# Kernel tuning notes

Hardware: AMD Instinct MI355X
Metric: run time of the kernel (lower is better)

The kernel has to match this reference:

```python
import jax, jax.numpy as jnp
import numpy as np

D_MODEL = 1024
H = 16
D_K = D_MODEL // H


def setup_inputs() -> dict:
    key = jax.random.key(0)
    ks = jax.random.split(key, 12)
    B, S = 4, 2048
    q = jax.random.normal(ks[0], (B, S, D_MODEL), jnp.float32)
    k = jax.random.normal(ks[1], (B, S, D_MODEL), jnp.float32)
    v = jax.random.normal(ks[2], (B, S, D_MODEL), jnp.float32)
    # causal mask, broadcastable to [B, H, S, S]; mask==0 positions are blocked
    mask = jnp.tril(jnp.ones((S, S), jnp.int32))[None, None]
    scale = 1.0 / np.sqrt(D_MODEL)
    Wq = jax.random.normal(ks[3], (D_MODEL, D_MODEL), jnp.float32) * scale
    bq = jax.random.normal(ks[4], (D_MODEL,), jnp.float32) * 0.02
    Wk = jax.random.normal(ks[5], (D_MODEL, D_MODEL), jnp.float32) * scale
    bk = jax.random.normal(ks[6], (D_MODEL,), jnp.float32) * 0.02
    Wv = jax.random.normal(ks[7], (D_MODEL, D_MODEL), jnp.float32) * scale
    bv = jax.random.normal(ks[8], (D_MODEL,), jnp.float32) * 0.02
    Wo = jax.random.normal(ks[9], (D_MODEL, D_MODEL), jnp.float32) * scale
    bo = jax.random.normal(ks[10], (D_MODEL,), jnp.float32) * 0.02
    return {"q": q, "k": k, "v": v, "mask": mask,
            "Wq": Wq, "bq": bq, "Wk": Wk, "bk": bk,
            "Wv": Wv, "bv": bv, "Wo": Wo, "bo": bo}


def reference(q, k, v, mask, Wq, bq, Wk, bk, Wv, bv, Wo, bo):
    B, S, _ = q.shape
    # linear projections (torch nn.Linear: x @ W.T + b)
    query = q @ Wq.T + bq
    key = k @ Wk.T + bk
    value = v @ Wv.T + bv
    # [B, S, D] -> [B, H, S, d_k]
    def split_heads(x):
        return x.reshape(B, S, H, D_K).transpose(0, 2, 1, 3)
    query, key, value = split_heads(query), split_heads(key), split_heads(value)
    # scaled dot-product attention, scores: [B, H, S, S]
    scores = jnp.einsum('bhqd,bhkd->bhqk', query, key) / np.sqrt(D_K)
    scores = jnp.where(mask == 0, jnp.float32(-1e9), scores)
    attn = jax.nn.softmax(scores, axis=-1)
    x = jnp.einsum('bhqk,bhkd->bhqd', attn, value)  # [B, H, S, d_k]
    x = x.transpose(0, 2, 1, 3).reshape(B, S, D_MODEL)
    return x @ Wo.T + bo
```

## Files before the change

kernel.cpp:

```cpp
#include <hip/hip_runtime.h>

#define DM 1024
#define SEQ 2048
#define NH 16
#define DK 64

typedef __bf16 bf16x8 __attribute__((ext_vector_type(8)));
typedef float f32x4 __attribute__((ext_vector_type(4)));

#define QSCALE 0.1803368801111244f

__device__ inline unsigned short f2bf(float f) {
    unsigned u = __float_as_uint(f);
    u += 0x7fffu + ((u >> 16) & 1u);
    return (unsigned short)(u >> 16);
}

__device__ inline unsigned pkbf(float lo, float hi) {
    union { __bf16 h[2]; unsigned u; } r;
    r.h[0] = (__bf16)lo; r.h[1] = (__bf16)hi;
    return r.u;
}

__global__ __launch_bounds__(256) void cvt_w(const float* __restrict__ s0,
                                             const float* __restrict__ s1,
                                             const float* __restrict__ s2,
                                             const float* __restrict__ s3,
                                             unsigned short* __restrict__ d0,
                                             unsigned short* __restrict__ d1,
                                             unsigned short* __restrict__ d2,
                                             unsigned short* __restrict__ d3) {
    const float* s;
    unsigned short* d;
    switch (blockIdx.y) {
        case 0: s = s0; d = d0; break;
        case 1: s = s1; d = d1; break;
        case 2: s = s2; d = d2; break;
        default: s = s3; d = d3; break;
    }
    int i = (blockIdx.x * 256 + threadIdx.x) * 4;
    float4 v = *(const float4*)(s + i);
    ushort4 o;
    o.x = f2bf(v.x); o.y = f2bf(v.y); o.z = f2bf(v.z); o.w = f2bf(v.w);
    *(ushort4*)(d + i) = o;
}

__global__ __launch_bounds__(512) void gemm_qkv(
    const float* __restrict__ Aq, const float* __restrict__ Ak,
    const float* __restrict__ Avv,
    const unsigned short* __restrict__ Wq2, const unsigned short* __restrict__ Wk2,
    const unsigned short* __restrict__ Wv2,
    const float* __restrict__ bq2, const float* __restrict__ bk2,
    const float* __restrict__ bv2,
    unsigned short* __restrict__ Cq, unsigned short* __restrict__ Ck,
    unsigned short* __restrict__ Cvt) {
    __shared__ unsigned short lds_a[128 * 64];
    __shared__ unsigned short lds_w[2][128 * 64];

    const int K = DM, N = DM;
    const int t = threadIdx.x;
    const int lane = t & 63;
    const int w = t >> 6;
    const int wr = w >> 1;
    const int wc = w & 1;
    const int seg = blockIdx.x >> 9;
    const int inner = blockIdx.x & 511;
    const int xcd = inner & 7;
    const int idx = inner >> 3;
    const int rowBase = (xcd * 8 + (idx >> 3)) * 128;
    const int colBase = (idx & 7) * 128;
    const int l15 = lane & 15;
    const int lg = lane >> 4;
    const int ar = t >> 2, aq = t & 3;
    const int NIT = K >> 6;

    const float* A = seg == 0 ? Aq : (seg == 1 ? Ak : Avv);
    const unsigned short* W = seg == 0 ? Wq2 : (seg == 1 ? Wk2 : Wv2);
    const float* bias = seg == 0 ? bq2 : (seg == 1 ? bk2 : bv2);

    f32x4 acc[2][4] = {};

    auto STAGE_W = [&](int kt, int buf) {
#pragma unroll
        for (int i = 0; i < 2; ++i) {
            const int row = (w * 2 + i) * 8 + (lane >> 3);
            const int sl = lane & 7;
            const unsigned short* src =
                W + (size_t)(colBase + row) * K + kt * 64 + ((sl ^ (row & 7)) * 8);
            __builtin_amdgcn_global_load_lds(src, &lds_w[buf][(w * 2 + i) * 512], 16, 0, 0);
        }
    };
    auto LOADA = [&](int kt, float4* rf) {
        const float* Af = A + (size_t)(rowBase + ar) * K + kt * 64 + aq * 16;
#pragma unroll
        for (int i = 0; i < 4; ++i) rf[i] = *(const float4*)(Af + i * 4);
    };
    auto WRITEA = [&](const float4* rf) {
#pragma unroll
        for (int i = 0; i < 2; ++i) {
            union { __bf16 h[8]; uint4 u; } pk;
            pk.h[0] = (__bf16)rf[2 * i].x; pk.h[1] = (__bf16)rf[2 * i].y;
            pk.h[2] = (__bf16)rf[2 * i].z; pk.h[3] = (__bf16)rf[2 * i].w;
            pk.h[4] = (__bf16)rf[2 * i + 1].x; pk.h[5] = (__bf16)rf[2 * i + 1].y;
            pk.h[6] = (__bf16)rf[2 * i + 1].z; pk.h[7] = (__bf16)rf[2 * i + 1].w;
            *(uint4*)&lds_a[ar * 64 + (((aq * 2 + i) ^ (ar & 7)) * 8)] = pk.u;
        }
    };
    auto COMPUTE = [&](int wbuf) {
#pragma unroll
        for (int kh = 0; kh < 2; ++kh) {
            bf16x8 af[2], wf[4];
#pragma unroll
            for (int m = 0; m < 2; ++m)
                af[m] = *(const bf16x8*)&lds_a[(wr * 32 + m * 16 + l15) * 64 +
                                               (((kh * 4 + lg) ^ (l15 & 7)) * 8)];
#pragma unroll
            for (int n = 0; n < 4; ++n)
                wf[n] = *(const bf16x8*)&lds_w[wbuf][(wc * 64 + n * 16 + l15) * 64 +
                                                    (((kh * 4 + lg) ^ (l15 & 7)) * 8)];
#pragma unroll
            for (int m = 0; m < 2; ++m)
#pragma unroll
                for (int n = 0; n < 4; ++n)
                    acc[m][n] = __builtin_amdgcn_mfma_f32_16x16x32_bf16(af[m], wf[n],
                                                                        acc[m][n], 0, 0, 0);
        }
    };

    float4 ra[4], rb[4];
    STAGE_W(0, 0);
    LOADA(0, ra);
    for (int kt = 0; kt < NIT; kt += 2) {
        if (kt + 1 < NIT) {
            STAGE_W(kt + 1, 1);
            LOADA(kt + 1, rb);
            asm volatile("s_waitcnt vmcnt(6)" ::: "memory");
        } else {
            asm volatile("s_waitcnt vmcnt(0)" ::: "memory");
        }
        WRITEA(ra);
        asm volatile("s_waitcnt lgkmcnt(0)" ::: "memory");
        __builtin_amdgcn_s_barrier();
        COMPUTE(0);
        __builtin_amdgcn_s_barrier();
        if (kt + 2 < NIT) {
            STAGE_W(kt + 2, 0);
            LOADA(kt + 2, ra);
            asm volatile("s_waitcnt vmcnt(6)" ::: "memory");
        } else {
            asm volatile("s_waitcnt vmcnt(0)" ::: "memory");
        }
        WRITEA(rb);
        asm volatile("s_waitcnt lgkmcnt(0)" ::: "memory");
        __builtin_amdgcn_s_barrier();
        COMPUTE(1);
        __builtin_amdgcn_s_barrier();
    }

    const float oscale = seg == 0 ? QSCALE : 1.0f;
#pragma unroll
    for (int m = 0; m < 2; ++m) {
        int row = rowBase + wr * 32 + m * 16 + lg * 4;
#pragma unroll
        for (int n = 0; n < 4; ++n) {
            int col = colBase + wc * 64 + n * 16 + l15;
            float bv = bias[col];
            if (seg == 2) {
                const int bh = (row >> 11) * NH + (col >> 6);
                const int dloc = col & 63;
                const int s = row & (SEQ - 1);
                ushort4 o;
                o.x = f2bf(acc[m][n][0] + bv);
                o.y = f2bf(acc[m][n][1] + bv);
                o.z = f2bf(acc[m][n][2] + bv);
                o.w = f2bf(acc[m][n][3] + bv);
                *(ushort4*)(Cvt + ((size_t)bh * DK + dloc) * SEQ + s) = o;
            } else {
                unsigned short* C = seg == 0 ? Cq : Ck;
#pragma unroll
                for (int j = 0; j < 4; ++j)
                    C[(size_t)(row + j) * N + col] = f2bf((acc[m][n][j] + bv) * oscale);
            }
        }
    }
}

__global__ __launch_bounds__(512) void gemm_out(const unsigned short* __restrict__ A,
                                                const unsigned short* __restrict__ W,
                                                const float* __restrict__ bias,
                                                float* __restrict__ C) {
    __shared__ unsigned short lds_a[2][128 * 64];
    __shared__ unsigned short lds_w[2][128 * 64];

    const int K = DM, N = DM;
    const int t = threadIdx.x;
    const int lane = t & 63;
    const int w = t >> 6;
    const int wr = w >> 1;
    const int wc = w & 1;
    const int bid = blockIdx.x;
    const int xcd = bid & 7;
    const int idx = bid >> 3;
    const int rowBase = (xcd * 8 + (idx >> 3)) * 128;
    const int colBase = (idx & 7) * 128;
    const int l15 = lane & 15;
    const int lg = lane >> 4;
    const int NIT = K >> 6;

    f32x4 acc[2][4] = {};

    auto STAGE = [&](const unsigned short* M0, unsigned short* ldsb, int kt) {
#pragma unroll
        for (int i = 0; i < 2; ++i) {
            const int row = (w * 2 + i) * 8 + (lane >> 3);
            const int sl = lane & 7;
            const unsigned short* src =
                M0 + (size_t)row * K + kt * 64 + ((sl ^ (row & 7)) * 8);
            __builtin_amdgcn_global_load_lds(src, ldsb + (w * 2 + i) * 512, 16, 0, 0);
        }
    };
    auto COMPUTE = [&](int buf) {
#pragma unroll
        for (int kh = 0; kh < 2; ++kh) {
            bf16x8 af[2], wf[4];
#pragma unroll
            for (int m = 0; m < 2; ++m)
                af[m] = *(const bf16x8*)&lds_a[buf][(wr * 32 + m * 16 + l15) * 64 +
                                                   (((kh * 4 + lg) ^ (l15 & 7)) * 8)];
#pragma unroll
            for (int n = 0; n < 4; ++n)
                wf[n] = *(const bf16x8*)&lds_w[buf][(wc * 64 + n * 16 + l15) * 64 +
                                                   (((kh * 4 + lg) ^ (l15 & 7)) * 8)];
#pragma unroll
            for (int m = 0; m < 2; ++m)
#pragma unroll
                for (int n = 0; n < 4; ++n)
                    acc[m][n] = __builtin_amdgcn_mfma_f32_16x16x32_bf16(af[m], wf[n],
                                                                        acc[m][n], 0, 0, 0);
        }
    };

    const unsigned short* Arow = A + (size_t)rowBase * K;
    const unsigned short* Wrow = W + (size_t)colBase * K;
    STAGE(Wrow, lds_w[0], 0);
    STAGE(Arow, lds_a[0], 0);
    for (int kt = 0; kt < NIT; ++kt) {
        const int cur = kt & 1;
        if (kt + 1 < NIT) {
            STAGE(Wrow, lds_w[cur ^ 1], kt + 1);
            STAGE(Arow, lds_a[cur ^ 1], kt + 1);
            asm volatile("s_waitcnt vmcnt(4)" ::: "memory");
        } else {
            asm volatile("s_waitcnt vmcnt(0)" ::: "memory");
        }
        __builtin_amdgcn_s_barrier();
        COMPUTE(cur);
        __builtin_amdgcn_s_barrier();
    }

#pragma unroll
    for (int m = 0; m < 2; ++m) {
        int row = rowBase + wr * 32 + m * 16 + lg * 4;
#pragma unroll
        for (int n = 0; n < 4; ++n) {
            int col = colBase + wc * 64 + n * 16 + l15;
            float bv = bias[col];
#pragma unroll
            for (int j = 0; j < 4; ++j)
                C[(size_t)(row + j) * N + col] = acc[m][n][j] + bv;
        }
    }
}

__global__ __launch_bounds__(256) void attn(const unsigned short* __restrict__ Q,
                                            const unsigned short* __restrict__ K,
                                            const unsigned short* __restrict__ Vt,
                                            unsigned short* __restrict__ X) {
    __shared__ unsigned short k_lds[2][64 * 64];
    __shared__ unsigned short v_lds[2][64 * 64];

    const int t = threadIdx.x;
    const int lane = t & 63;
    const int w = t >> 6;
    const int l15 = lane & 15, lg = lane >> 4;
    const int c4 = (lane >> 4) & 1, c5 = (lane >> 5) & 1;

    const int orig = blockIdx.x;
    const int flat = (orig & 7) * 128 + (orig >> 3);
    const int bh = flat >> 4;
    const int pr = flat & 15;
    const int b = bh >> 4, h = bh & 15;

    const unsigned short* Qb = Q + (size_t)b * SEQ * DM + h * DK;
    const unsigned short* Kb = K + (size_t)b * SEQ * DM + h * DK;
    const unsigned short* Vb = Vt + (size_t)bh * DK * SEQ;

    const int sr = t >> 3;
    const int sc8 = (t & 7) * 8;
    const int sxo = (sr & 7) * 8;
    const int xork = (l15 & 7) * 8;

    union { unsigned short us[8]; bf16x8 v; } ou;
#pragma unroll
    for (int i = 0; i < 8; ++i) ou.us[i] = 0x3F80;
    const bf16x8 onesf = ou.v;

    bf16x8 kr0, kr1, vr0, vr1;
    int gp = 0;

    auto LOADT = [&](int kv0) {
        kr0 = *(const bf16x8*)(Kb + (size_t)(kv0 + sr) * DM + sc8);
        kr1 = *(const bf16x8*)(Kb + (size_t)(kv0 + 32 + sr) * DM + sc8);
        vr0 = *(const bf16x8*)(Vb + (size_t)sr * SEQ + kv0 + sc8);
        vr1 = *(const bf16x8*)(Vb + (size_t)(32 + sr) * SEQ + kv0 + sc8);
    };

    LOADT(0);

    for (int task = 0; task < 2; ++task) {
        const int qt = task ? 31 - pr : pr;
        const int qrow0 = qt * 64 + w * 16;
        const int qg = qrow0 + l15;

        const bf16x8 qf0 = *(const bf16x8*)(Qb + (size_t)(qrow0 + l15) * DM + lg * 8);
        const bf16x8 qf1 = *(const bf16x8*)(Qb + (size_t)(qrow0 + l15) * DM + lg * 8 + 32);

        f32x4 acc[4] = {};
        f32x4 accS = {};
        const int nt = qt + 1;

        for (int tile = 0; tile < nt; ++tile) {
            const int kv0 = tile << 6;
            unsigned short* kl = k_lds[gp & 1];
            unsigned short* vl = v_lds[gp & 1];
            *(bf16x8*)&kl[sr * 64 + (sc8 ^ sxo)] = kr0;
            *(bf16x8*)&kl[(sr + 32) * 64 + (sc8 ^ sxo)] = kr1;
            *(bf16x8*)&vl[sr * 64 + (sc8 ^ sxo)] = vr0;
            *(bf16x8*)&vl[(sr + 32) * 64 + (sc8 ^ sxo)] = vr1;
            __syncthreads();

            if (tile + 1 < nt)
                LOADT((tile + 1) << 6);
            else if (task == 0)
                LOADT(0);

            f32x4 st[4];
#pragma unroll
            for (int s = 0; s < 4; ++s) {
                const int rb2 = (s * 16 + l15) * 64;
                bf16x8 ka = *(const bf16x8*)&kl[rb2 + ((lg * 8) ^ xork)];
                bf16x8 kb2 = *(const bf16x8*)&kl[rb2 + ((32 + lg * 8) ^ xork)];
                f32x4 z = {};
                z = __builtin_amdgcn_mfma_f32_16x16x32_bf16(ka, qf0, z, 0, 0, 0);
                st[s] = __builtin_amdgcn_mfma_f32_16x16x32_bf16(kb2, qf1, z, 0, 0, 0);
            }

            bf16x8 vf[4][2];
#pragma unroll
            for (int d = 0; d < 4; ++d) {
                const int rb2 = (d * 16 + l15) * 64;
                vf[d][0] = *(const bf16x8*)&vl[rb2 + ((lg * 8) ^ xork)];
                vf[d][1] = *(const bf16x8*)&vl[rb2 + ((32 + lg * 8) ^ xork)];
            }

            float ps[16];
            if (kv0 + 63 > qrow0) {
#pragma unroll
                for (int s = 0; s < 4; ++s)
#pragma unroll
                    for (int j = 0; j < 4; ++j) {
                        const bool ok = kv0 + s * 16 + 4 * lg + j <= qg;
                        ps[s * 4 + j] = ok ? exp2f(st[s][j]) : 0.0f;
                    }
            } else {
#pragma unroll
                for (int s = 0; s < 4; ++s)
#pragma unroll
                    for (int j = 0; j < 4; ++j)
                        ps[s * 4 + j] = exp2f(st[s][j]);
            }

            bf16x8 pf[2];
#pragma unroll
            for (int hh = 0; hh < 2; ++hh) {
                const float* p8 = &ps[hh * 8];
                unsigned wsp[2][2];
#pragma unroll
                for (int s = 0; s < 2; ++s)
#pragma unroll
                    for (int p2 = 0; p2 < 2; ++p2)
                        wsp[s][p2] = pkbf(p8[s * 4 + 2 * p2], p8[s * 4 + 2 * p2 + 1]);
                unsigned n0[2], n1[2];
#pragma unroll
                for (int p2 = 0; p2 < 2; ++p2) {
                    unsigned snd = c5 ? wsp[0][p2] : wsp[1][p2];
                    unsigned exch = __shfl_xor((int)snd, 32, 64);
                    n0[p2] = c5 ? exch : wsp[0][p2];
                    n1[p2] = c5 ? wsp[1][p2] : exch;
                }
                unsigned f0[2], f1[2];
#pragma unroll
                for (int p2 = 0; p2 < 2; ++p2) {
                    unsigned snd = c4 ? n0[p2] : n1[p2];
                    unsigned exch = __shfl_xor((int)snd, 16, 64);
                    f0[p2] = c4 ? exch : n0[p2];
                    f1[p2] = c4 ? n1[p2] : exch;
                }
                union { unsigned u[4]; bf16x8 v; } pu;
                pu.u[0] = f0[0]; pu.u[1] = f0[1]; pu.u[2] = f1[0]; pu.u[3] = f1[1];
                pf[hh] = pu.v;
            }

#pragma unroll
            for (int d = 0; d < 4; ++d) {
                acc[d] = __builtin_amdgcn_mfma_f32_16x16x32_bf16(vf[d][0], pf[0], acc[d], 0, 0, 0);
                acc[d] = __builtin_amdgcn_mfma_f32_16x16x32_bf16(vf[d][1], pf[1], acc[d], 0, 0, 0);
            }
            accS = __builtin_amdgcn_mfma_f32_16x16x32_bf16(onesf, pf[0], accS, 0, 0, 0);
            accS = __builtin_amdgcn_mfma_f32_16x16x32_bf16(onesf, pf[1], accS, 0, 0, 0);
            gp++;
        }

        const float inv = 1.0f / accS[0];
#pragma unroll
        for (int d = 0; d < 4; ++d) {
            ushort4 o;
            o.x = f2bf(acc[d][0] * inv);
            o.y = f2bf(acc[d][1] * inv);
            o.z = f2bf(acc[d][2] * inv);
            o.w = f2bf(acc[d][3] * inv);
            *(ushort4*)&X[(size_t)(b * SEQ + qg) * DM + h * DK + d * 16 + 4 * lg] = o;
        }
    }
}

extern "C" void kernel_launch(void* const* d_in, const int* in_sizes, int n_in,
                              void* d_out, int out_size, void* d_ws, size_t ws_size,
                              hipStream_t stream) {
    const float* q  = (const float*)d_in[0];
    const float* k  = (const float*)d_in[1];
    const float* v  = (const float*)d_in[2];
    const float* Wq = (const float*)d_in[4];
    const float* bq = (const float*)d_in[5];
    const float* Wk = (const float*)d_in[6];
    const float* bk = (const float*)d_in[7];
    const float* Wv = (const float*)d_in[8];
    const float* bv = (const float*)d_in[9];
    const float* Wo = (const float*)d_in[10];
    const float* bo = (const float*)d_in[11];

    const size_t NEL = (size_t)4 * SEQ * DM;
    const size_t WEL = (size_t)DM * DM;
    unsigned short* Qp  = (unsigned short*)d_ws;
    unsigned short* Kp  = Qp + NEL;
    unsigned short* Vp  = Kp + NEL;
    unsigned short* Vt  = Vp + NEL;
    unsigned short* Wob = Vt + NEL;
    unsigned short* Xp  = Vp;
    unsigned short* Wqb = (unsigned short*)d_out;
    unsigned short* Wkb = Wqb + WEL;
    unsigned short* Wvb = Wkb + WEL;

    hipLaunchKernelGGL(cvt_w, dim3(1024, 4), dim3(256), 0, stream, Wq, Wk, Wv, Wo,
                       Wqb, Wkb, Wvb, Wob);
    hipLaunchKernelGGL(gemm_qkv, dim3(1536), dim3(512), 0, stream, q, k, v,
                       Wqb, Wkb, Wvb, bq, bk, bv, Qp, Kp, Vt);
    hipLaunchKernelGGL(attn, dim3(1024), dim3(256), 0, stream, Qp, Kp, Vt, Xp);
    hipLaunchKernelGGL(gemm_out, dim3(512), dim3(512), 0, stream, Xp, Wob, bo,
                       (float*)d_out);
}
```

Measured before the change: 203.7 us.

## Deepen A-operand register prefetch to three stages in QKV projection GEMM

Measured after the change: 201.7 us. Within noise of the previous version (-1.0%).

```diff
diff --git a/kernel.cpp b/kernel.cpp
--- a/kernel.cpp
+++ b/kernel.cpp
@@ -72,7 +72,6 @@
     const int l15 = lane & 15;
     const int lg = lane >> 4;
     const int ar = t >> 2, aq = t & 3;
-    const int NIT = K >> 6;
 
     const float* A = seg == 0 ? Aq : (seg == 1 ? Ak : Avv);
     const unsigned short* W = seg == 0 ? Wq2 : (seg == 1 ? Wk2 : Wv2);
@@ -127,33 +126,26 @@
         }
     };
 
-    float4 ra[4], rb[4];
+    float4 rs[3][4];
     STAGE_W(0, 0);
-    LOADA(0, ra);
-    for (int kt = 0; kt < NIT; kt += 2) {
-        if (kt + 1 < NIT) {
-            STAGE_W(kt + 1, 1);
-            LOADA(kt + 1, rb);
+    LOADA(0, rs[0]);
+    LOADA(1, rs[1]);
+    LOADA(2, rs[2]);
+#pragma unroll
+    for (int kt = 0; kt < 16; ++kt) {
+        if (kt + 1 < 16) STAGE_W(kt + 1, (kt + 1) & 1);
+        if (kt < 14) {
+            asm volatile("s_waitcnt vmcnt(10)" ::: "memory");
+        } else if (kt == 14) {
             asm volatile("s_waitcnt vmcnt(6)" ::: "memory");
         } else {
             asm volatile("s_waitcnt vmcnt(0)" ::: "memory");
         }
-        WRITEA(ra);
+        WRITEA(rs[kt % 3]);
+        if (kt + 3 < 16) LOADA(kt + 3, rs[kt % 3]);
         asm volatile("s_waitcnt lgkmcnt(0)" ::: "memory");
         __builtin_amdgcn_s_barrier();
-        COMPUTE(0);
-        __builtin_amdgcn_s_barrier();
-        if (kt + 2 < NIT) {
-            STAGE_W(kt + 2, 0);
-            LOADA(kt + 2, ra);
-            asm volatile("s_waitcnt vmcnt(6)" ::: "memory");
-        } else {
-            asm volatile("s_waitcnt vmcnt(0)" ::: "memory");
-        }
-        WRITEA(rb);
-        asm volatile("s_waitcnt lgkmcnt(0)" ::: "memory");
-        __builtin_amdgcn_s_barrier();
-        COMPUTE(1);
+        COMPUTE(kt & 1);
         __builtin_amdgcn_s_barrier();
     }
 
```
